# Kernel optimization log

Hardware: AMD Instinct MI355X
Metric: run time of the kernel (lower is better)

The kernel has to match this reference:

```python
import jax, jax.numpy as jnp
import numpy as np

K = 128
HEADS = 8
B = 4
T = 2048


def setup_inputs() -> dict:
    key = jax.random.key(0)
    ks = jax.random.split(key, 6)
    x = jax.random.normal(ks[0], (B, T, K), dtype=jnp.float32)
    s = 1.0 / np.sqrt(K)
    # torch nn.Linear weights are (out_features, in_features)
    Wq = jax.random.uniform(ks[1], (HEADS * K, K), dtype=jnp.float32, minval=-s, maxval=s)
    Wk = jax.random.uniform(ks[2], (HEADS * K, K), dtype=jnp.float32, minval=-s, maxval=s)
    Wv = jax.random.uniform(ks[3], (HEADS * K, K), dtype=jnp.float32, minval=-s, maxval=s)
    su = 1.0 / np.sqrt(HEADS * K)
    Wu = jax.random.uniform(ks[4], (K, HEADS * K), dtype=jnp.float32, minval=-su, maxval=su)
    bu = jax.random.uniform(ks[5], (K,), dtype=jnp.float32, minval=-su, maxval=su)
    return {"x": x, "Wq": Wq, "Wk": Wk, "Wv": Wv, "Wu": Wu, "bu": bu}


def reference(x, Wq, Wk, Wv, Wu, bu):
    b, t, k = x.shape
    h = HEADS
    # project: Linear(k, k*h) then view(b,t,h,k); weight reshaped to (h, k_out, k_in)
    q = jnp.einsum('btk,hdk->bhtd', x, Wq.reshape(h, k, k))
    kk = jnp.einsum('btk,hdk->bhtd', x, Wk.reshape(h, k, k))
    v = jnp.einsum('btk,hdk->bhtd', x, Wv.reshape(h, k, k))
    scale = jnp.asarray(k, x.dtype) ** 0.25
    q = q / scale
    kk = kk / scale
    dot = jnp.einsum('bhtd,bhsd->bhts', q, kk)  # [b,h,t,t]
    att = jax.nn.softmax(dot, axis=-1)
    out = jnp.einsum('bhts,bhsd->bhtd', att, v)  # [b,h,t,k]
    out = out.transpose(0, 2, 1, 3).reshape(b, t, h * k)
    return out @ Wu.T + bu
```

## Files before the change

kernel.cpp:

```cpp
#include <hip/hip_runtime.h>
#include <cmath>

namespace {

constexpr int HEADS = 8;
constexpr int Bn = 4;
constexpr int Tn = 2048;
constexpr int Dn = 128;
constexpr float Q_PRESCALE = 0.1275174340f;

typedef _Float16 half8 __attribute__((ext_vector_type(8)));
typedef _Float16 half4 __attribute__((ext_vector_type(4)));
typedef float f32x4 __attribute__((ext_vector_type(4)));

__global__ __launch_bounds__(256) void cast_kernel(
    const float* __restrict__ x, const float* __restrict__ Wq, const float* __restrict__ Wk,
    const float* __restrict__ Wv, const float* __restrict__ Wu, _Float16* __restrict__ xh,
    _Float16* __restrict__ WH) {
  const int idx = blockIdx.x * 256 + threadIdx.x;
  const size_t base = (size_t)idx * 8;
  const float* src;
  _Float16* dst;
  if (base < 1048576) {
    src = x + base;
    dst = xh + base;
  } else {
    const size_t r = base - 1048576;
    const int s = (int)(r >> 17);
    src = ((s == 0) ? Wq : (s == 1) ? Wk : (s == 2) ? Wv : Wu) + (r & 131071);
    dst = WH + r;
  }
  const float4 a = *reinterpret_cast<const float4*>(src);
  const float4 b = *reinterpret_cast<const float4*>(src + 4);
  half8 h;
  h[0] = (_Float16)a.x; h[1] = (_Float16)a.y; h[2] = (_Float16)a.z; h[3] = (_Float16)a.w;
  h[4] = (_Float16)b.x; h[5] = (_Float16)b.y; h[6] = (_Float16)b.z; h[7] = (_Float16)b.w;
  *reinterpret_cast<half8*>(dst) = h;
}

__global__ __launch_bounds__(256, 4) void proj_kernel(const _Float16* __restrict__ xh,
                                                      const _Float16* __restrict__ WH,
                                                      _Float16* __restrict__ Qh,
                                                      _Float16* __restrict__ Kh,
                                                      _Float16* __restrict__ Vt) {
  __shared__ _Float16 sB[128 * 136];
  const int tid = threadIdx.x;
  const int w = tid >> 6, lane = tid & 63, quad = lane >> 4, l16 = lane & 15;
  const int m0 = blockIdx.x * 128;
  const int n0 = blockIdx.y * 128;

#pragma unroll
  for (int it = 0; it < 8; ++it) {
    const int fid = tid + it * 256;
    const int r = fid >> 4, g = fid & 15;
    const half8 v = *reinterpret_cast<const half8*>(WH + (size_t)(n0 + r) * 128 + g * 8);
    const int p = g ^ (r & 15);
    *reinterpret_cast<half8*>(sB + r * 128 + p * 8) = v;
  }

  half8 af[2][4];
  const _Float16* xp = xh + (size_t)(m0 + w * 32 + l16) * 128 + quad * 8;
#pragma unroll
  for (int mt = 0; mt < 2; ++mt)
#pragma unroll
    for (int kk = 0; kk < 4; ++kk)
      af[mt][kk] = *reinterpret_cast<const half8*>(xp + mt * 16 * 128 + kk * 32);

  __syncthreads();

  f32x4 acc[2][8];
#pragma unroll
  for (int mt = 0; mt < 2; ++mt)
#pragma unroll
    for (int nt = 0; nt < 8; ++nt) acc[mt][nt] = (f32x4){0.f, 0.f, 0.f, 0.f};

#pragma unroll
  for (int kk = 0; kk < 4; ++kk)
#pragma unroll
    for (int nt = 0; nt < 8; ++nt) {
      const int r = nt * 16 + l16;
      const int p = (kk * 4 + quad) ^ l16;
      const half8 bf = *reinterpret_cast<const half8*>(sB + r * 128 + p * 8);
      acc[0][nt] = __builtin_amdgcn_mfma_f32_16x16x32_f16(af[0][kk], bf, acc[0][nt], 0, 0, 0);
      acc[1][nt] = __builtin_amdgcn_mfma_f32_16x16x32_f16(af[1][kk], bf, acc[1][nt], 0, 0, 0);
    }

  const int sel = n0 >> 10;
  const int h = (n0 >> 7) & 7;
  const int b = m0 >> 11;
  const int t0b = m0 & 2047;
  const int bh = b * HEADS + h;
  const float scale = (sel == 0) ? Q_PRESCALE : 1.0f;

  __syncthreads();

  if (sel < 2) {
#pragma unroll
    for (int mt = 0; mt < 2; ++mt)
#pragma unroll
      for (int nt = 0; nt < 8; ++nt)
#pragma unroll
        for (int r = 0; r < 4; ++r)
          sB[(w * 32 + mt * 16 + quad * 4 + r) * 136 + nt * 16 + l16] =
              (_Float16)(acc[mt][nt][r] * scale);
  } else {
#pragma unroll
    for (int mt = 0; mt < 2; ++mt)
#pragma unroll
      for (int nt = 0; nt < 8; ++nt)
#pragma unroll
        for (int r = 0; r < 4; ++r)
          sB[(nt * 16 + l16) * 136 + w * 32 + mt * 16 + quad * 4 + r] = (_Float16)acc[mt][nt][r];
  }
  __syncthreads();

  _Float16* dstbase;
  size_t rstride;
  if (sel == 0) {
    dstbase = Qh + ((size_t)bh * Tn + t0b) * Dn;
    rstride = Dn;
  } else if (sel == 1) {
    dstbase = Kh + ((size_t)bh * Tn + t0b) * Dn;
    rstride = Dn;
  } else {
    dstbase = Vt + ((size_t)bh * Dn) * Tn + t0b;
    rstride = Tn;
  }
#pragma unroll
  for (int it = 0; it < 8; ++it) {
    const int fid = tid + it * 256;
    const int r = fid >> 4, g = fid & 15;
    const half8 v = *reinterpret_cast<const half8*>(sB + r * 136 + g * 8);
    *reinterpret_cast<half8*>(dstbase + (size_t)r * rstride + g * 8) = v;
  }
}

__global__ __launch_bounds__(256, 2) void flash_kernel(const _Float16* __restrict__ Qh,
                                                       const _Float16* __restrict__ Kh,
                                                       const _Float16* __restrict__ Vt,
                                                       _Float16* __restrict__ Obh) {
  __shared__ _Float16 sK[64 * 128];
  __shared__ _Float16 sV[128 * 64];
  __shared__ _Float16 sP[4][32 * 64];
  __shared__ float sL[4][2][16];

  const int tid = threadIdx.x;
  const int w = tid >> 6;
  const int lane = tid & 63;
  const int quad = lane >> 4;
  const int l16 = lane & 15;
  const int qt = blockIdx.x;
  const int bh = blockIdx.y;

  half8 qf[2][4];
#pragma unroll
  for (int qg = 0; qg < 2; ++qg) {
    const _Float16* Qp =
        Qh + ((size_t)bh * Tn + qt * 128 + w * 32 + qg * 16 + l16) * Dn + quad * 8;
#pragma unroll
    for (int kk = 0; kk < 4; ++kk) qf[qg][kk] = *reinterpret_cast<const half8*>(Qp + kk * 32);
  }

  const _Float16* Kp = Kh + (size_t)bh * Tn * Dn;
  const _Float16* Vp = Vt + (size_t)bh * Dn * Tn;
  _Float16* sPw = sP[w];

  f32x4 o[2][8];
#pragma unroll
  for (int qg = 0; qg < 2; ++qg)
#pragma unroll
    for (int nt = 0; nt < 8; ++nt) o[qg][nt] = (f32x4){0.f, 0.f, 0.f, 0.f};
  float lsum[2] = {0.f, 0.f};

  half8 kreg[4], vreg[4];
  const int kr = tid >> 4, kg = tid & 15;
  const int vr = tid >> 3, vg = tid & 7;
#pragma unroll
  for (int it = 0; it < 4; ++it) {
    kreg[it] = *reinterpret_cast<const half8*>(Kp + (size_t)(kr + it * 16) * Dn + kg * 8);
    vreg[it] = *reinterpret_cast<const half8*>(Vp + (size_t)(vr + it * 32) * Tn + vg * 8);
  }

  for (int st = 0; st < Tn / 64; ++st) {
    __syncthreads();
#pragma unroll
    for (int it = 0; it < 4; ++it) {
      const int r = kr + it * 16;
      const int p = kg ^ (r & 15);
      *reinterpret_cast<half8*>(sK + r * 128 + p * 8) = kreg[it];
      const int rv = vr + it * 32;
      const int pv = vg ^ ((rv & 7) ^ ((rv >> 1) & 4));
      *reinterpret_cast<half8*>(sV + rv * 64 + pv * 8) = vreg[it];
    }
    if (st + 1 < Tn / 64) {
      const _Float16* knext = Kp + (size_t)(st + 1) * 64 * Dn;
      const _Float16* vnext = Vp + (st + 1) * 64;
#pragma unroll
      for (int it = 0; it < 4; ++it) {
        kreg[it] = *reinterpret_cast<const half8*>(knext + (size_t)(kr + it * 16) * Dn + kg * 8);
        vreg[it] = *reinterpret_cast<const half8*>(vnext + (size_t)(vr + it * 32) * Tn + vg * 8);
      }
    }
    __syncthreads();

    f32x4 s_t[2][4];
#pragma unroll
    for (int qg = 0; qg < 2; ++qg)
#pragma unroll
      for (int j = 0; j < 4; ++j) s_t[qg][j] = (f32x4){0.f, 0.f, 0.f, 0.f};
#pragma unroll
    for (int kk = 0; kk < 4; ++kk)
#pragma unroll
      for (int j = 0; j < 4; ++j) {
        const int p = (kk * 4 + quad) ^ l16;
        const half8 kf = *reinterpret_cast<const half8*>(sK + (j * 16 + l16) * 128 + p * 8);
        s_t[0][j] = __builtin_amdgcn_mfma_f32_16x16x32_f16(kf, qf[0][kk], s_t[0][j], 0, 0, 0);
        s_t[1][j] = __builtin_amdgcn_mfma_f32_16x16x32_f16(kf, qf[1][kk], s_t[1][j], 0, 0, 0);
      }

#pragma unroll
    for (int qg = 0; qg < 2; ++qg)
#pragma unroll
      for (int j = 0; j < 4; ++j) {
        f32x4 e;
        e[0] = __builtin_amdgcn_exp2f(s_t[qg][j][0]);
        e[1] = __builtin_amdgcn_exp2f(s_t[qg][j][1]);
        e[2] = __builtin_amdgcn_exp2f(s_t[qg][j][2]);
        e[3] = __builtin_amdgcn_exp2f(s_t[qg][j][3]);
        lsum[qg] += (e[0] + e[1]) + (e[2] + e[3]);
        half4 h4;
        h4[0] = (_Float16)e[0]; h4[1] = (_Float16)e[1];
        h4[2] = (_Float16)e[2]; h4[3] = (_Float16)e[3];
        const int g = j * 2 + (quad >> 1);
        const int p = g ^ (l16 & 7);
        *reinterpret_cast<half4*>(sPw + (qg * 16 + l16) * 64 + p * 8 + (quad & 1) * 4) = h4;
      }

#pragma unroll
    for (int kk2 = 0; kk2 < 2; ++kk2) {
      half8 pf[2];
#pragma unroll
      for (int qg = 0; qg < 2; ++qg) {
        const int pA = (kk2 * 4 + quad) ^ (l16 & 7);
        pf[qg] = *reinterpret_cast<const half8*>(sPw + (qg * 16 + l16) * 64 + pA * 8);
      }
#pragma unroll
      for (int nt = 0; nt < 8; ++nt) {
        const int r = nt * 16 + l16;
        const int pV = (kk2 * 4 + quad) ^ ((r & 7) ^ ((r >> 1) & 4));
        const half8 vf = *reinterpret_cast<const half8*>(sV + r * 64 + pV * 8);
        o[0][nt] = __builtin_amdgcn_mfma_f32_16x16x32_f16(pf[0], vf, o[0][nt], 0, 0, 0);
        o[1][nt] = __builtin_amdgcn_mfma_f32_16x16x32_f16(pf[1], vf, o[1][nt], 0, 0, 0);
      }
    }
  }

#pragma unroll
  for (int qg = 0; qg < 2; ++qg) {
    float ls = lsum[qg];
    ls += __shfl_xor(ls, 16);
    ls += __shfl_xor(ls, 32);
    if (quad == 0) sL[w][qg][l16] = 1.0f / ls;
  }
  const int b = bh >> 3, h = bh & 7;
#pragma unroll
  for (int qg = 0; qg < 2; ++qg) {
    const f32x4 inv4 = *reinterpret_cast<const f32x4*>(&sL[w][qg][quad * 4]);
#pragma unroll
    for (int r = 0; r < 4; ++r) {
      const size_t trow =
          (size_t)(b * Tn + qt * 128 + w * 32 + qg * 16 + quad * 4 + r) * (HEADS * Dn);
#pragma unroll
      for (int nt = 0; nt < 8; ++nt)
        Obh[trow + h * Dn + nt * 16 + l16] = (_Float16)(o[qg][nt][r] * inv4[r]);
    }
  }
}

__global__ __launch_bounds__(256, 4) void outproj_kernel(const _Float16* __restrict__ Obh,
                                                         const _Float16* __restrict__ Wuh,
                                                         const float* __restrict__ bu,
                                                         float* __restrict__ out) {
  __shared__ float sR[4 * 32 * 128];
  const int tid = threadIdx.x;
  const int w = tid >> 6, lane = tid & 63, quad = lane >> 4, l16 = lane & 15;
  const int r0 = blockIdx.x * 32;

  f32x4 acc[2][8];
#pragma unroll
  for (int mt = 0; mt < 2; ++mt)
#pragma unroll
    for (int nt = 0; nt < 8; ++nt) acc[mt][nt] = (f32x4){0.f, 0.f, 0.f, 0.f};

  const _Float16* ap = Obh + (size_t)(r0 + l16) * 1024 + w * 256 + quad * 8;
  const _Float16* bp = Wuh + (size_t)l16 * 1024 + w * 256 + quad * 8;

#pragma unroll
  for (int kk = 0; kk < 8; ++kk) {
    const half8 a0 = *reinterpret_cast<const half8*>(ap + kk * 32);
    const half8 a1 = *reinterpret_cast<const half8*>(ap + 16 * 1024 + kk * 32);
#pragma unroll
    for (int nt = 0; nt < 8; ++nt) {
      const half8 bf = *reinterpret_cast<const half8*>(bp + (size_t)nt * 16 * 1024 + kk * 32);
      acc[0][nt] = __builtin_amdgcn_mfma_f32_16x16x32_f16(a0, bf, acc[0][nt], 0, 0, 0);
      acc[1][nt] = __builtin_amdgcn_mfma_f32_16x16x32_f16(a1, bf, acc[1][nt], 0, 0, 0);
    }
  }

#pragma unroll
  for (int mt = 0; mt < 2; ++mt)
#pragma unroll
    for (int nt = 0; nt < 8; ++nt)
#pragma unroll
      for (int r = 0; r < 4; ++r)
        sR[w * 4096 + (mt * 16 + quad * 4 + r) * 128 + nt * 16 + l16] = acc[mt][nt][r];
  __syncthreads();

#pragma unroll
  for (int it = 0; it < 16; ++it) {
    const int idx = tid + it * 256;
    const int row = idx >> 7, col = idx & 127;
    const float v = sR[idx] + sR[4096 + idx] + sR[8192 + idx] + sR[12288 + idx] + bu[col];
    out[(size_t)(r0 + row) * Dn + col] = v;
  }
}

}

extern "C" void kernel_launch(void* const* d_in, const int* in_sizes, int n_in, void* d_out,
                              int out_size, void* d_ws, size_t ws_size, hipStream_t stream) {
  (void)in_sizes; (void)n_in; (void)out_size; (void)ws_size;
  const float* x = (const float*)d_in[0];
  const float* Wq = (const float*)d_in[1];
  const float* Wk = (const float*)d_in[2];
  const float* Wv = (const float*)d_in[3];
  const float* Wu = (const float*)d_in[4];
  const float* bu = (const float*)d_in[5];
  float* out = (float*)d_out;

  constexpr size_t NE = (size_t)Bn * HEADS * Tn * Dn;
  char* ws = (char*)d_ws;
  _Float16* xh = (_Float16*)ws;
  _Float16* WH = (_Float16*)(ws + 2097152);
  _Float16* Qh = (_Float16*)(ws + 4194304);
  _Float16* Kh = (_Float16*)(ws + 4194304 + NE * 2);
  _Float16* Vt = (_Float16*)(ws + 4194304 + NE * 4);
  _Float16* Obh = (_Float16*)(ws + 4194304 + NE * 6);
  _Float16* Wuh = WH + 393216;

  cast_kernel<<<dim3(768), 256, 0, stream>>>(x, Wq, Wk, Wv, Wu, xh, WH);
  proj_kernel<<<dim3(64, 24), 256, 0, stream>>>(xh, WH, Qh, Kh, Vt);
  flash_kernel<<<dim3(16, 32), 256, 0, stream>>>(Qh, Kh, Vt, Obh);
  outproj_kernel<<<dim3(256), 256, 0, stream>>>(Obh, Wuh, bu, out);
}
```

Baseline: 173.2 us.

## Use 8 waves per flash block with 16 query rows per wave

```diff
diff --git a/kernel.cpp b/kernel.cpp
--- a/kernel.cpp
+++ b/kernel.cpp
@@ -135,14 +135,14 @@
   }
 }
 
-__global__ __launch_bounds__(256, 2) void flash_kernel(const _Float16* __restrict__ Qh,
+__global__ __launch_bounds__(512, 4) void flash_kernel(const _Float16* __restrict__ Qh,
                                                        const _Float16* __restrict__ Kh,
                                                        const _Float16* __restrict__ Vt,
                                                        _Float16* __restrict__ Obh) {
   __shared__ _Float16 sK[64 * 128];
   __shared__ _Float16 sV[128 * 64];
-  __shared__ _Float16 sP[4][32 * 64];
-  __shared__ float sL[4][2][16];
+  __shared__ _Float16 sP[8][16 * 64];
+  __shared__ float sL[8][16];
 
   const int tid = threadIdx.x;
   const int w = tid >> 6;
@@ -152,43 +152,39 @@
   const int qt = blockIdx.x;
   const int bh = blockIdx.y;
 
-  half8 qf[2][4];
-#pragma unroll
-  for (int qg = 0; qg < 2; ++qg) {
-    const _Float16* Qp =
-        Qh + ((size_t)bh * Tn + qt * 128 + w * 32 + qg * 16 + l16) * Dn + quad * 8;
-#pragma unroll
-    for (int kk = 0; kk < 4; ++kk) qf[qg][kk] = *reinterpret_cast<const half8*>(Qp + kk * 32);
+  half8 qf[4];
+  {
+    const _Float16* Qp = Qh + ((size_t)bh * Tn + qt * 128 + w * 16 + l16) * Dn + quad * 8;
+#pragma unroll
+    for (int kk = 0; kk < 4; ++kk) qf[kk] = *reinterpret_cast<const half8*>(Qp + kk * 32);
   }
 
   const _Float16* Kp = Kh + (size_t)bh * Tn * Dn;
   const _Float16* Vp = Vt + (size_t)bh * Dn * Tn;
   _Float16* sPw = sP[w];
 
-  f32x4 o[2][8];
-#pragma unroll
-  for (int qg = 0; qg < 2; ++qg)
-#pragma unroll
-    for (int nt = 0; nt < 8; ++nt) o[qg][nt] = (f32x4){0.f, 0.f, 0.f, 0.f};
-  float lsum[2] = {0.f, 0.f};
-
-  half8 kreg[4], vreg[4];
+  f32x4 o[8];
+#pragma unroll
+  for (int nt = 0; nt < 8; ++nt) o[nt] = (f32x4){0.f, 0.f, 0.f, 0.f};
+  float lsum = 0.f;
+
+  half8 kreg[2], vreg[2];
   const int kr = tid >> 4, kg = tid & 15;
   const int vr = tid >> 3, vg = tid & 7;
 #pragma unroll
-  for (int it = 0; it < 4; ++it) {
-    kreg[it] = *reinterpret_cast<const half8*>(Kp + (size_t)(kr + it * 16) * Dn + kg * 8);
-    vreg[it] = *reinterpret_cast<const half8*>(Vp + (size_t)(vr + it * 32) * Tn + vg * 8);
+  for (int it = 0; it < 2; ++it) {
+    kreg[it] = *reinterpret_cast<const half8*>(Kp + (size_t)(kr + it * 32) * Dn + kg * 8);
+    vreg[it] = *reinterpret_cast<const half8*>(Vp + (size_t)(vr + it * 64) * Tn + vg * 8);
   }
 
   for (int st = 0; st < Tn / 64; ++st) {
     __syncthreads();
 #pragma unroll
-    for (int it = 0; it < 4; ++it) {
-      const int r = kr + it * 16;
+    for (int it = 0; it < 2; ++it) {
+      const int r = kr + it * 32;
       const int p = kg ^ (r & 15);
       *reinterpret_cast<half8*>(sK + r * 128 + p * 8) = kreg[it];
-      const int rv = vr + it * 32;
+      const int rv = vr + it * 64;
       const int pv = vg ^ ((rv & 7) ^ ((rv >> 1) & 4));
       *reinterpret_cast<half8*>(sV + rv * 64 + pv * 8) = vreg[it];
     }
@@ -196,83 +192,71 @@
       const _Float16* knext = Kp + (size_t)(st + 1) * 64 * Dn;
       const _Float16* vnext = Vp + (st + 1) * 64;
 #pragma unroll
-      for (int it = 0; it < 4; ++it) {
-        kreg[it] = *reinterpret_cast<const half8*>(knext + (size_t)(kr + it * 16) * Dn + kg * 8);
-        vreg[it] = *reinterpret_cast<const half8*>(vnext + (size_t)(vr + it * 32) * Tn + vg * 8);
+      for (int it = 0; it < 2; ++it) {
+        kreg[it] = *reinterpret_cast<const half8*>(knext + (size_t)(kr + it * 32) * Dn + kg * 8);
+        vreg[it] = *reinterpret_cast<const half8*>(vnext + (size_t)(vr + it * 64) * Tn + vg * 8);
       }
     }
     __syncthreads();
 
-    f32x4 s_t[2][4];
-#pragma unroll
-    for (int qg = 0; qg < 2; ++qg)
-#pragma unroll
-      for (int j = 0; j < 4; ++j) s_t[qg][j] = (f32x4){0.f, 0.f, 0.f, 0.f};
+    f32x4 s_t[4];
+#pragma unroll
+    for (int j = 0; j < 4; ++j) s_t[j] = (f32x4){0.f, 0.f, 0.f, 0.f};
 #pragma unroll
     for (int kk = 0; kk < 4; ++kk)
 #pragma unroll
       for (int j = 0; j < 4; ++j) {
         const int p = (kk * 4 + quad) ^ l16;
         const half8 kf = *reinterpret_cast<const half8*>(sK + (j * 16 + l16) * 128 + p * 8);
-        s_t[0][j] = __builtin_amdgcn_mfma_f32_16x16x32_f16(kf, qf[0][kk], s_t[0][j], 0, 0, 0);
-        s_t[1][j] = __builtin_amdgcn_mfma_f32_16x16x32_f16(kf, qf[1][kk], s_t[1][j], 0, 0, 0);
+        s_t[j] = __builtin_amdgcn_mfma_f32_16x16x32_f16(kf, qf[kk], s_t[j], 0, 0, 0);
       }
 
 #pragma unroll
-    for (int qg = 0; qg < 2; ++qg)
-#pragma unroll
-      for (int j = 0; j < 4; ++j) {
-        f32x4 e;
-        e[0] = __builtin_amdgcn_exp2f(s_t[qg][j][0]);
-        e[1] = __builtin_amdgcn_exp2f(s_t[qg][j][1]);
-        e[2] = __builtin_amdgcn_exp2f(s_t[qg][j][2]);
-        e[3] = __builtin_amdgcn_exp2f(s_t[qg][j][3]);
-        lsum[qg] += (e[0] + e[1]) + (e[2] + e[3]);
-        half4 h4;
-        h4[0] = (_Float16)e[0]; h4[1] = (_Float16)e[1];
-        h4[2] = (_Float16)e[2]; h4[3] = (_Float16)e[3];
-        const int g = j * 2 + (quad >> 1);
-        const int p = g ^ (l16 & 7);
-        *reinterpret_cast<half4*>(sPw + (qg * 16 + l16) * 64 + p * 8 + (quad & 1) * 4) = h4;
-      }
+    for (int j = 0; j < 4; ++j) {
+      f32x4 e;
+      e[0] = __builtin_amdgcn_exp2f(s_t[j][0]);
+      e[1] = __builtin_amdgcn_exp2f(s_t[j][1]);
+      e[2] = __builtin_amdgcn_exp2f(s_t[j][2]);
+      e[3] = __builtin_amdgcn_exp2f(s_t[j][3]);
+      lsum += (e[0] + e[1]) + (e[2] + e[3]);
+      half4 h4;
+      h4[0] = (_Float16)e[0]; h4[1] = (_Float16)e[1];
+      h4[2] = (_Float16)e[2]; h4[3] = (_Float16)e[3];
+      const int g = j * 2 + (quad >> 1);
+      const int p = g ^ (l16 & 7);
+      *reinterpret_cast<half4*>(sPw + l16 * 64 + p * 8 + (quad & 1) * 4) = h4;
+    }
 
 #pragma unroll
     for (int kk2 = 0; kk2 < 2; ++kk2) {
-      half8 pf[2];
-#pragma unroll
-      for (int qg = 0; qg < 2; ++qg) {
-        const int pA = (kk2 * 4 + quad) ^ (l16 & 7);
-        pf[qg] = *reinterpret_cast<const half8*>(sPw + (qg * 16 + l16) * 64 + pA * 8);
-      }
+      const int pA = (kk2 * 4 + quad) ^ (l16 & 7);
+      const half8 pf = *reinterpret_cast<const half8*>(sPw + l16 * 64 + pA * 8);
 #pragma unroll
       for (int nt = 0; nt < 8; ++nt) {
         const int r = nt * 16 + l16;
         const int pV = (kk2 * 4 + quad) ^ ((r & 7) ^ ((r >> 1) & 4));
         const half8 vf = *reinterpret_cast<const half8*>(sV + r * 64 + pV * 8);
-        o[0][nt] = __builtin_amdgcn_mfma_f32_16x16x32_f16(pf[0], vf, o[0][nt], 0, 0, 0);
-        o[1][nt] = __builtin_amdgcn_mfma_f32_16x16x32_f16(pf[1], vf, o[1][nt], 0, 0, 0);
+        o[nt] = __builtin_amdgcn_mfma_f32_16x16x32_f16(pf, vf, o[nt], 0, 0, 0);
       }
     }
   }
 
-#pragma unroll
-  for (int qg = 0; qg < 2; ++qg) {
-    float ls = lsum[qg];
+  {
+    float ls = lsum;
     ls += __shfl_xor(ls, 16);
     ls += __shfl_xor(ls, 32);
-    if (quad == 0) sL[w][qg][l16] = 1.0f / ls;
+    if (quad == 0) sL[w][l16] = 1.0f / ls;
   }
   const int b = bh >> 3, h = bh & 7;
-#pragma unroll
-  for (int qg = 0; qg < 2; ++qg) {
-    const f32x4 inv4 = *reinterpret_cast<const f32x4*>(&sL[w][qg][quad * 4]);
+  {
+    const f32x4 inv4 = *reinterpret_cast<const f32x4*>(&sL[w][quad * 4]);
 #pragma unroll
     for (int r = 0; r < 4; ++r) {
       const size_t trow =
-          (size_t)(b * Tn + qt * 128 + w * 32 + qg * 16 + quad * 4 + r) * (HEADS * Dn);
+          (size_t)(b * Tn + qt * 128 + w * 16 + quad * 4 + r) * (HEADS * Dn);
 #pragma unroll
       for (int nt = 0; nt < 8; ++nt)
-        Obh[trow + h * Dn + nt * 16 + l16] = (_Float16)(o[qg][nt][r] * inv4[r]);
+        Obh[trow + h * Dn + nt * 16 + l16] = (_Float16)(o[nt][r] * inv4[r]);
     }
   }
 }
@@ -350,6 +334,6 @@
 
   cast_kernel<<<dim3(768), 256, 0, stream>>>(x, Wq, Wk, Wv, Wu, xh, WH);
   proj_kernel<<<dim3(64, 24), 256, 0, stream>>>(xh, WH, Qh, Kh, Vt);
-  flash_kernel<<<dim3(16, 32), 256, 0, stream>>>(Qh, Kh, Vt, Obh);
+  flash_kernel<<<dim3(16, 32), 512, 0, stream>>>(Qh, Kh, Vt, Obh);
   outproj_kernel<<<dim3(256), 256, 0, stream>>>(Obh, Wuh, bu, out);
 }
```

New measurement: 176.6 us. No clear change (+1.9%).

## Double-buffer K/V shared tiles and software-pipeline QK^T with PV

Applied to the files above, without the earlier changes.

```diff
diff --git a/kernel.cpp b/kernel.cpp
--- a/kernel.cpp
+++ b/kernel.cpp
@@ -139,10 +139,9 @@
                                                        const _Float16* __restrict__ Kh,
                                                        const _Float16* __restrict__ Vt,
                                                        _Float16* __restrict__ Obh) {
-  __shared__ _Float16 sK[64 * 128];
-  __shared__ _Float16 sV[128 * 64];
+  __shared__ _Float16 sK[2][64 * 128];
+  __shared__ _Float16 sV[2][128 * 64];
   __shared__ _Float16 sP[4][32 * 64];
-  __shared__ float sL[4][2][16];
 
   const int tid = threadIdx.x;
   const int w = tid >> 6;
@@ -151,6 +150,7 @@
   const int l16 = lane & 15;
   const int qt = blockIdx.x;
   const int bh = blockIdx.y;
+  constexpr int NT = Tn / 64;
 
   half8 qf[2][4];
 #pragma unroll
@@ -175,97 +175,135 @@
   half8 kreg[4], vreg[4];
   const int kr = tid >> 4, kg = tid & 15;
   const int vr = tid >> 3, vg = tid & 7;
+
 #pragma unroll
   for (int it = 0; it < 4; ++it) {
     kreg[it] = *reinterpret_cast<const half8*>(Kp + (size_t)(kr + it * 16) * Dn + kg * 8);
     vreg[it] = *reinterpret_cast<const half8*>(Vp + (size_t)(vr + it * 32) * Tn + vg * 8);
   }
-
-  for (int st = 0; st < Tn / 64; ++st) {
-    __syncthreads();
-#pragma unroll
-    for (int it = 0; it < 4; ++it) {
-      const int r = kr + it * 16;
-      const int p = kg ^ (r & 15);
-      *reinterpret_cast<half8*>(sK + r * 128 + p * 8) = kreg[it];
-      const int rv = vr + it * 32;
-      const int pv = vg ^ ((rv & 7) ^ ((rv >> 1) & 4));
-      *reinterpret_cast<half8*>(sV + rv * 64 + pv * 8) = vreg[it];
-    }
-    if (st + 1 < Tn / 64) {
-      const _Float16* knext = Kp + (size_t)(st + 1) * 64 * Dn;
-      const _Float16* vnext = Vp + (st + 1) * 64;
+#pragma unroll
+  for (int it = 0; it < 4; ++it) {
+    const int r = kr + it * 16;
+    const int p = kg ^ (r & 15);
+    *reinterpret_cast<half8*>(sK[0] + r * 128 + p * 8) = kreg[it];
+    const int rv = vr + it * 32;
+    const int pv = vg ^ ((rv & 7) ^ ((rv >> 1) & 4));
+    *reinterpret_cast<half8*>(sV[0] + rv * 64 + pv * 8) = vreg[it];
+  }
+#pragma unroll
+  for (int it = 0; it < 4; ++it) {
+    kreg[it] = *reinterpret_cast<const half8*>(Kp + (size_t)(64 + kr + it * 16) * Dn + kg * 8);
+    vreg[it] = *reinterpret_cast<const half8*>(Vp + (size_t)(vr + it * 32) * Tn + 64 + vg * 8);
+  }
+  __syncthreads();
+
+  f32x4 s_t[2][4];
+#pragma unroll
+  for (int qg = 0; qg < 2; ++qg)
+#pragma unroll
+    for (int j = 0; j < 4; ++j) s_t[qg][j] = (f32x4){0.f, 0.f, 0.f, 0.f};
+#pragma unroll
+  for (int kk = 0; kk < 4; ++kk)
+#pragma unroll
+    for (int j = 0; j < 4; ++j) {
+      const int p = (kk * 4 + quad) ^ l16;
+      const half8 kf = *reinterpret_cast<const half8*>(sK[0] + (j * 16 + l16) * 128 + p * 8);
+      s_t[0][j] = __builtin_amdgcn_mfma_f32_16x16x32_f16(kf, qf[0][kk], s_t[0][j], 0, 0, 0);
+      s_t[1][j] = __builtin_amdgcn_mfma_f32_16x16x32_f16(kf, qf[1][kk], s_t[1][j], 0, 0, 0);
+    }
+
+  for (int st = 0; st < NT; ++st) {
+    const int cur = st & 1, nxt = cur ^ 1;
+
+    if (st + 1 < NT) {
+#pragma unroll
+      for (int it = 0; it < 4; ++it) {
+        const int r = kr + it * 16;
+        const int p = kg ^ (r & 15);
+        *reinterpret_cast<half8*>(sK[nxt] + r * 128 + p * 8) = kreg[it];
+        const int rv = vr + it * 32;
+        const int pv = vg ^ ((rv & 7) ^ ((rv >> 1) & 4));
+        *reinterpret_cast<half8*>(sV[nxt] + rv * 64 + pv * 8) = vreg[it];
+      }
+    }
+    if (st + 2 < NT) {
+      const _Float16* knext = Kp + (size_t)(st + 2) * 64 * Dn;
+      const _Float16* vnext = Vp + (st + 2) * 64;
 #pragma unroll
       for (int it = 0; it < 4; ++it) {
         kreg[it] = *reinterpret_cast<const half8*>(knext + (size_t)(kr + it * 16) * Dn + kg * 8);
         vreg[it] = *reinterpret_cast<const half8*>(vnext + (size_t)(vr + it * 32) * Tn + vg * 8);
       }
     }
-    __syncthreads();
-
-    f32x4 s_t[2][4];
-#pragma unroll
-    for (int qg = 0; qg < 2; ++qg)
-#pragma unroll
-      for (int j = 0; j < 4; ++j) s_t[qg][j] = (f32x4){0.f, 0.f, 0.f, 0.f};
-#pragma unroll
-    for (int kk = 0; kk < 4; ++kk)
-#pragma unroll
-      for (int j = 0; j < 4; ++j) {
-        const int p = (kk * 4 + quad) ^ l16;
-        const half8 kf = *reinterpret_cast<const half8*>(sK + (j * 16 + l16) * 128 + p * 8);
-        s_t[0][j] = __builtin_amdgcn_mfma_f32_16x16x32_f16(kf, qf[0][kk], s_t[0][j], 0, 0, 0);
-        s_t[1][j] = __builtin_amdgcn_mfma_f32_16x16x32_f16(kf, qf[1][kk], s_t[1][j], 0, 0, 0);
-      }
-
-#pragma unroll
-    for (int qg = 0; qg < 2; ++qg)
-#pragma unroll
-      for (int j = 0; j < 4; ++j) {
-        f32x4 e;
-        e[0] = __builtin_amdgcn_exp2f(s_t[qg][j][0]);
-        e[1] = __builtin_amdgcn_exp2f(s_t[qg][j][1]);
-        e[2] = __builtin_amdgcn_exp2f(s_t[qg][j][2]);
-        e[3] = __builtin_amdgcn_exp2f(s_t[qg][j][3]);
-        lsum[qg] += (e[0] + e[1]) + (e[2] + e[3]);
-        half4 h4;
-        h4[0] = (_Float16)e[0]; h4[1] = (_Float16)e[1];
-        h4[2] = (_Float16)e[2]; h4[3] = (_Float16)e[3];
-        const int g = j * 2 + (quad >> 1);
-        const int p = g ^ (l16 & 7);
-        *reinterpret_cast<half4*>(sPw + (qg * 16 + l16) * 64 + p * 8 + (quad & 1) * 4) = h4;
-      }
-
-#pragma unroll
-    for (int kk2 = 0; kk2 < 2; ++kk2) {
+
+#pragma unroll
+    for (int h = 0; h < 2; ++h) {
+#pragma unroll
+      for (int qg = 0; qg < 2; ++qg)
+#pragma unroll
+        for (int jj = 0; jj < 2; ++jj) {
+          const int j = h * 2 + jj;
+          f32x4 e;
+          e[0] = __builtin_amdgcn_exp2f(s_t[qg][j][0]);
+          e[1] = __builtin_amdgcn_exp2f(s_t[qg][j][1]);
+          e[2] = __builtin_amdgcn_exp2f(s_t[qg][j][2]);
+          e[3] = __builtin_amdgcn_exp2f(s_t[qg][j][3]);
+          lsum[qg] += (e[0] + e[1]) + (e[2] + e[3]);
+          half4 h4;
+          h4[0] = (_Float16)e[0]; h4[1] = (_Float16)e[1];
+          h4[2] = (_Float16)e[2]; h4[3] = (_Float16)e[3];
+          const int g = j * 2 + (quad >> 1);
+          const int p = g ^ (l16 & 7);
+          *reinterpret_cast<half4*>(sPw + (qg * 16 + l16) * 64 + p * 8 + (quad & 1) * 4) = h4;
+        }
       half8 pf[2];
 #pragma unroll
       for (int qg = 0; qg < 2; ++qg) {
-        const int pA = (kk2 * 4 + quad) ^ (l16 & 7);
+        const int pA = (h * 4 + quad) ^ (l16 & 7);
         pf[qg] = *reinterpret_cast<const half8*>(sPw + (qg * 16 + l16) * 64 + pA * 8);
       }
 #pragma unroll
       for (int nt = 0; nt < 8; ++nt) {
         const int r = nt * 16 + l16;
-        const int pV = (kk2 * 4 + quad) ^ ((r & 7) ^ ((r >> 1) & 4));
-        const half8 vf = *reinterpret_cast<const half8*>(sV + r * 64 + pV * 8);
+        const int pV = (h * 4 + quad) ^ ((r & 7) ^ ((r >> 1) & 4));
+        const half8 vf = *reinterpret_cast<const half8*>(sV[cur] + r * 64 + pV * 8);
         o[0][nt] = __builtin_amdgcn_mfma_f32_16x16x32_f16(pf[0], vf, o[0][nt], 0, 0, 0);
         o[1][nt] = __builtin_amdgcn_mfma_f32_16x16x32_f16(pf[1], vf, o[1][nt], 0, 0, 0);
       }
     }
-  }
-
+
+    __syncthreads();
+
+    if (st + 1 < NT) {
+#pragma unroll
+      for (int qg = 0; qg < 2; ++qg)
+#pragma unroll
+        for (int j = 0; j < 4; ++j) s_t[qg][j] = (f32x4){0.f, 0.f, 0.f, 0.f};
+#pragma unroll
+      for (int kk = 0; kk < 4; ++kk)
+#pragma unroll
+        for (int j = 0; j < 4; ++j) {
+          const int p = (kk * 4 + quad) ^ l16;
+          const half8 kf =
+              *reinterpret_cast<const half8*>(sK[nxt] + (j * 16 + l16) * 128 + p * 8);
+          s_t[0][j] = __builtin_amdgcn_mfma_f32_16x16x32_f16(kf, qf[0][kk], s_t[0][j], 0, 0, 0);
+          s_t[1][j] = __builtin_amdgcn_mfma_f32_16x16x32_f16(kf, qf[1][kk], s_t[1][j], 0, 0, 0);
+        }
+    }
+  }
+
+  float* sLw = reinterpret_cast<float*>(sPw);
 #pragma unroll
   for (int qg = 0; qg < 2; ++qg) {
     float ls = lsum[qg];
     ls += __shfl_xor(ls, 16);
     ls += __shfl_xor(ls, 32);
-    if (quad == 0) sL[w][qg][l16] = 1.0f / ls;
+    if (quad == 0) sLw[qg * 16 + l16] = 1.0f / ls;
   }
   const int b = bh >> 3, h = bh & 7;
 #pragma unroll
   for (int qg = 0; qg < 2; ++qg) {
-    const f32x4 inv4 = *reinterpret_cast<const f32x4*>(&sL[w][qg][quad * 4]);
+    const f32x4 inv4 = *reinterpret_cast<const f32x4*>(sLw + qg * 16 + quad * 4);
 #pragma unroll
     for (int r = 0; r < 4; ++r) {
       const size_t trow =
```

Result: faster. 168.5 us (-2.7%).
